# Performance work log

Hardware: AMD Instinct MI355X
Metric: run time of the kernel (lower is better)

## Reference

```python
import jax, jax.numpy as jnp
import numpy as np

N = 4096
IN_C = 256
F = 256          # num_filter
C = 40           # label_dim
KP1 = 3          # K+1 Chebyshev orders (K=2 hardcoded in forward)
E = 131072
TWO_PI = 2.0 * np.pi


def build_Lc(edges, q, edge_weight, n):
    """Conjugate of the normalized magnetic Laplacian (max_eigen=2 => L = -A_n * exp(i*Theta)).
    We return conj(L) because the original code swaps L.real/L.imag when feeding `process`,
    which is algebraically O_i = i * conj(T_i(L))."""
    row, col = edges[0], edges[1]
    A = jnp.zeros((n, n), jnp.float32).at[row, col].add(edge_weight)  # duplicates sum, as in coo_matrix
    A_sym = 0.5 * (A + A.T)
    d = A_sym.sum(axis=0)
    d = jnp.where(d == 0, 1.0, d)
    dinv = d ** -0.5
    A_n = dinv[:, None] * A_sym * dinv[None, :]
    Theta = TWO_PI * q * (A - A.T)
    # conj(L) = -A_n * exp(-i*Theta)
    return (-A_n).astype(jnp.complex64) * jnp.exp(-1j * Theta.astype(jnp.complex64))


def cheb_layer(Lc, Xr, Xi, W, b):
    """One ChebConv_Qin_Direct layer. Output = sum_i (i * T_i(conj(L)) @ Xc) @ W_i + bias,
    which reproduces the real/imag-swapped `process` of the original module."""
    Xc = (Xr + 1j * Xi).astype(jnp.complex64)      # [N, d]
    Z0 = Xc
    Z1 = Lc @ Xc                                   # sparse-equivalent spmm, dense here
    Z2 = 2.0 * (Lc @ Z1) - Z0                      # Chebyshev recursion T2 = 2 L T1 - T0
    Yc = 1j * (Z0 @ W[0].astype(jnp.complex64)
               + Z1 @ W[1].astype(jnp.complex64)
               + Z2 @ W[2].astype(jnp.complex64))  # [N, out]
    return Yc.real + b, Yc.imag + b


def setup_inputs() -> dict:
    key = jax.random.key(0)
    k = jax.random.split(key, 8)
    stdv1 = 1.0 / np.sqrt(F)
    return {
        "real": jax.random.normal(k[0], (N, IN_C), jnp.float32),
        "imag": jax.random.normal(k[1], (N, IN_C), jnp.float32),
        "edges": jax.random.randint(k[2], (2, E), 0, N),
        "q": jnp.float32(0.25),
        "edge_weight": jax.random.uniform(k[3], (E,), jnp.float32),
        "W1": jax.random.uniform(k[4], (KP1, IN_C, F), jnp.float32, -stdv1, stdv1),
        "b1": jnp.zeros((1, F), jnp.float32),
        "W2": jax.random.uniform(k[5], (KP1, F, F), jnp.float32, -stdv1, stdv1),
        "b2": jnp.zeros((1, F), jnp.float32),
        "Wc": jax.random.normal(k[6], (C, 2 * F), jnp.float32) * (1.0 / np.sqrt(2 * F)),
        "bc": jnp.zeros((C,), jnp.float32),
    }


def reference(real, imag, edges, q, edge_weight, W1, b1, W2, b2, Wc, bc):
    n = real.shape[0]
    Lc = build_Lc(edges, q, edge_weight, n)        # same L is rebuilt each layer in the original
    r, i = cheb_layer(Lc, real, imag, W1, b1)
    r, i = cheb_layer(Lc, r, i, W2, b2)            # activation=False, dropout=False
    x = jnp.concatenate([r, i], axis=-1)           # [N, 2F]
    logits = x @ Wc.T + bc                         # Conv1d(kernel_size=1) == linear
    return jax.nn.log_softmax(logits, axis=-1)     # [N, C]
```

## Files before the change

### kernel.cpp

```cpp
#include <hip/hip_runtime.h>
#include <cmath>

#define N_NODES 4096
#define FDIM    256
#define CDIM    40
#define NEDGE   131072
#define CAP     256
#define HBITS   20
#define HSIZE   (1 << HBITS)
#define TWO_PI_F 6.28318530717958647692f

typedef __bf16 bf16;
typedef __bf16 bf16x2 __attribute__((ext_vector_type(2)));
typedef __bf16 bf16x4 __attribute__((ext_vector_type(4)));
typedef __bf16 bf16x8 __attribute__((ext_vector_type(8)));
typedef float  f32x4  __attribute__((ext_vector_type(4)));

static constexpr size_t NF = (size_t)N_NODES * FDIM;

struct __align__(16) Entry { float lr, li; int col, pad; };

__device__ __forceinline__ void gld_lds16(const bf16* g, bf16* s) {
    __builtin_amdgcn_global_load_lds(
        (const __attribute__((address_space(1))) void*)g,
        (__attribute__((address_space(3))) void*)s,
        16, 0, 0);
}

__device__ __forceinline__ unsigned cell_hash(unsigned cell) {
    return (cell * 2654435761u) >> (32 - HBITS);
}

__global__ void hash_insert(const int* __restrict__ edges,
                            const float* __restrict__ ew,
                            int* __restrict__ hkey, float* __restrict__ hval,
                            float* __restrict__ rowsum, float* __restrict__ colsum) {
    int e = blockIdx.x * blockDim.x + threadIdx.x;
    if (e >= NEDGE) return;
    int r = edges[e], c = edges[NEDGE + e];
    float wv = ew[e];
    atomicAdd(rowsum + r, wv);
    atomicAdd(colsum + c, wv);
    unsigned cell = (unsigned)r * N_NODES + c;
    unsigned h = cell_hash(cell);
    for (;;) {
        int old = atomicCAS(hkey + h, 0, (int)(cell + 1));
        if (old == 0 || old == (int)(cell + 1)) { atomicAdd(hval + h, wv); break; }
        h = (h + 1) & (HSIZE - 1);
    }
}

__global__ __launch_bounds__(256) void hash_to_ell(
    const int* __restrict__ hkey, const float* __restrict__ hval,
    const float* __restrict__ rowsum, const float* __restrict__ colsum,
    const float* __restrict__ qptr,
    int* __restrict__ cnt, Entry* __restrict__ ent) {
    int h = blockIdx.x * 256 + threadIdx.x;
    int k = hkey[h];
    if (k == 0) return;
    unsigned cell = (unsigned)(k - 1);
    int i = cell >> 12, j = cell & 4095;
    float a = hval[h];
    float b = 0.f;
    bool mirror = false;
    if (i == j) { b = a; mirror = true; }
    else {
        unsigned mcell = (unsigned)j * N_NODES + i;
        unsigned hh = cell_hash(mcell);
        for (;;) {
            int kk = hkey[hh];
            if (kk == (int)(mcell + 1)) { b = hval[hh]; mirror = true; break; }
            if (kk == 0) break;
            hh = (hh + 1) & (HSIZE - 1);
        }
    }
    float di = 0.5f * (rowsum[i] + colsum[i]); if (di == 0.f) di = 1.f;
    float dj = 0.5f * (rowsum[j] + colsum[j]); if (dj == 0.f) dj = 1.f;
    float an = 0.5f * (a + b) / sqrtf(di * dj);
    float s, c;
    sincosf(TWO_PI_F * qptr[0] * (a - b), &s, &c);
    int pos = atomicAdd(cnt + i, 1);
    if (pos < CAP) {
        Entry en; en.lr = -an * c; en.li = an * s; en.col = j; en.pad = 0;
        ent[(size_t)i * CAP + pos] = en;
    }
    if (!mirror) {
        int pos2 = atomicAdd(cnt + j, 1);
        if (pos2 < CAP) {
            Entry en; en.lr = -an * c; en.li = -an * s; en.col = i; en.pad = 0;
            ent[(size_t)j * CAP + pos2] = en;
        }
    }
}

__global__ __launch_bounds__(256) void cast_in2(const float* __restrict__ Xr,
                                                const float* __restrict__ Xi,
                                                bf16* __restrict__ Xr16,
                                                bf16* __restrict__ Xi16,
                                                bf16* __restrict__ XC) {
    int idx = blockIdx.x * 256 + threadIdx.x;
    float vr = Xr[idx], vi = Xi[idx];
    Xr16[idx] = (bf16)vr; Xi16[idx] = (bf16)vi;
    bf16x2 p; p[0] = (bf16)vr; p[1] = (bf16)vi;
    ((bf16x2*)XC)[idx] = p;
}

#define NWT (256 * 768)
__global__ __launch_bounds__(256) void cast_weights(
    const float* __restrict__ W1, const float* __restrict__ W2,
    const float* __restrict__ Wc,
    bf16* __restrict__ W1t, bf16* __restrict__ W2t, bf16* __restrict__ Wcb) {
    int idx = blockIdx.x * 256 + threadIdx.x;
    if (idx < 2 * NWT) {
        const float* W = (idx < NWT) ? W1 : W2;
        bf16* Wt = (idx < NWT) ? W1t : W2t;
        int id = (idx < NWT) ? idx : idx - NWT;
        int nout = id / 768, kk = id - nout * 768;
        int o = kk >> 8, k = kk & 255;
        Wt[id] = (bf16)W[((size_t)o * 256 + k) * 256 + nout];
    } else {
        int id = idx - 2 * NWT;
        if (id < 48 * 512) {
            int row = id >> 9, k = id & 511;
            Wcb[id] = (row < CDIM) ? (bf16)Wc[row * 512 + k] : (bf16)0.f;
        }
    }
}

__global__ __launch_bounds__(256) void spmm_k(
    const int* __restrict__ cnt, const Entry* __restrict__ ent,
    const bf16* __restrict__ XC,
    const bf16* __restrict__ C0C,
    float alpha, float beta,
    bf16* __restrict__ Zr, bf16* __restrict__ Zi, bf16* __restrict__ ZC)
{
    __shared__ f32x4 redR[3][64];
    __shared__ f32x4 redI[3][64];

    const int wave = threadIdx.x >> 6, lane = threadIdx.x & 63;
    const int row = blockIdx.x;
    int n1 = cnt[row]; if (n1 > CAP) n1 = CAP;
    const Entry* erow = ent + (size_t)row * CAP;

    float ar[4] = {}, ai[4] = {};
    int e = wave;
    for (; e + 12 < n1; e += 16) {
        Entry e0 = erow[e];
        Entry e1 = erow[e + 4];
        Entry e2 = erow[e + 8];
        Entry e3 = erow[e + 12];
        bf16x8 x0 = *(const bf16x8*)&XC[(size_t)(e0.col & 4095) * 512 + lane * 8];
        bf16x8 x1 = *(const bf16x8*)&XC[(size_t)(e1.col & 4095) * 512 + lane * 8];
        bf16x8 x2 = *(const bf16x8*)&XC[(size_t)(e2.col & 4095) * 512 + lane * 8];
        bf16x8 x3 = *(const bf16x8*)&XC[(size_t)(e3.col & 4095) * 512 + lane * 8];
        #pragma unroll
        for (int c = 0; c < 4; ++c) {
            float xr, xi;
            xr = (float)x0[2 * c]; xi = (float)x0[2 * c + 1];
            ar[c] += e0.lr * xr - e0.li * xi;  ai[c] += e0.lr * xi + e0.li * xr;
            xr = (float)x1[2 * c]; xi = (float)x1[2 * c + 1];
            ar[c] += e1.lr * xr - e1.li * xi;  ai[c] += e1.lr * xi + e1.li * xr;
            xr = (float)x2[2 * c]; xi = (float)x2[2 * c + 1];
            ar[c] += e2.lr * xr - e2.li * xi;  ai[c] += e2.lr * xi + e2.li * xr;
            xr = (float)x3[2 * c]; xi = (float)x3[2 * c + 1];
            ar[c] += e3.lr * xr - e3.li * xi;  ai[c] += e3.lr * xi + e3.li * xr;
        }
    }
    for (; e < n1; e += 4) {
        Entry e0 = erow[e];
        bf16x8 x0 = *(const bf16x8*)&XC[(size_t)(e0.col & 4095) * 512 + lane * 8];
        #pragma unroll
        for (int c = 0; c < 4; ++c) {
            float xr0 = (float)x0[2 * c], xi0 = (float)x0[2 * c + 1];
            ar[c] += e0.lr * xr0 - e0.li * xi0;
            ai[c] += e0.lr * xi0 + e0.li * xr0;
        }
    }

    if (wave != 0) {
        f32x4 r, i;
        #pragma unroll
        for (int c = 0; c < 4; ++c) { r[c] = ar[c]; i[c] = ai[c]; }
        redR[wave - 1][lane] = r;
        redI[wave - 1][lane] = i;
    }
    __syncthreads();
    if (wave != 0) return;

    #pragma unroll
    for (int w = 0; w < 3; ++w) {
        f32x4 r = redR[w][lane], i = redI[w][lane];
        #pragma unroll
        for (int c = 0; c < 4; ++c) { ar[c] += r[c]; ai[c] += i[c]; }
    }

    float vr[4], vi[4];
    if (beta != 0.f) {
        bf16x8 c0 = *(const bf16x8*)&C0C[(size_t)row * 512 + lane * 8];
        #pragma unroll
        for (int c = 0; c < 4; ++c) {
            vr[c] = alpha * ar[c] + beta * (float)c0[2 * c];
            vi[c] = alpha * ai[c] + beta * (float)c0[2 * c + 1];
        }
    } else {
        #pragma unroll
        for (int c = 0; c < 4; ++c) { vr[c] = alpha * ar[c]; vi[c] = alpha * ai[c]; }
    }
    size_t base = (size_t)row * FDIM + lane * 4;
    bf16x4 pr, pi;
    #pragma unroll
    for (int c = 0; c < 4; ++c) { pr[c] = (bf16)vr[c]; pi[c] = (bf16)vi[c]; }
    *(bf16x4*)&Zr[base] = pr;
    *(bf16x4*)&Zi[base] = pi;
    if (ZC) {
        bf16x8 o;
        #pragma unroll
        for (int c = 0; c < 4; ++c) { o[2 * c] = pr[c]; o[2 * c + 1] = pi[c]; }
        *(bf16x8*)&ZC[(size_t)row * 512 + lane * 8] = o;
    }
}

__global__ __launch_bounds__(256) void wapply_mfma(
    const bf16* __restrict__ Z0r, const bf16* __restrict__ Z0i,
    const bf16* __restrict__ Z1r, const bf16* __restrict__ Z1i,
    const bf16* __restrict__ Z2r, const bf16* __restrict__ Z2i,
    const bf16* __restrict__ Wt,
    const float* __restrict__ bias,
    float* __restrict__ O32r, float* __restrict__ O32i,
    bf16* __restrict__ O16r_r, bf16* __restrict__ O16r_i,
    bf16* __restrict__ OC)
{
    __shared__ __align__(16) bf16 sZr[64 * 32];
    __shared__ __align__(16) bf16 sZi[64 * 32];
    __shared__ __align__(16) bf16 sW [64 * 32];

    const int tid  = threadIdx.x;
    const int wave = tid >> 6;
    const int lane = tid & 63;
    const int rowBase = blockIdx.y * 64;
    const int colBase = blockIdx.x * 64;

    const int srow = lane >> 2;
    const int skc  = (lane & 3) * 8;

    f32x4 accSr[2][2] = {}, accSi[2][2] = {};
    const int wm = wave & 1, wn = wave >> 1;
    const int fr = lane & 15;
    const int fk = (lane >> 4) * 8;

    for (int kb = 0; kb < 3 * FDIM; kb += 32) {
        int order = kb >> 8;
        int kloc  = kb & 255;
        if (wave == 0 || wave == 1) {
            const bf16* z;
            if (wave == 0) z = (order == 0) ? Z0r : (order == 1) ? Z1r : Z2r;
            else           z = (order == 0) ? Z0i : (order == 1) ? Z1i : Z2i;
            bf16* s = (wave == 0) ? sZr : sZi;
            const bf16* g = z + (size_t)(rowBase + srow) * FDIM + kloc + skc;
            #pragma unroll
            for (int t = 0; t < 4; ++t)
                gld_lds16(g + (size_t)t * 16 * FDIM, s + t * 512);
        } else if (wave == 2) {
            const bf16* g = Wt + (size_t)(colBase + srow) * 768 + kb + skc;
            #pragma unroll
            for (int t = 0; t < 4; ++t)
                gld_lds16(g + (size_t)t * 16 * 768, sW + t * 512);
        }
        __syncthreads();

        bf16x8 zr[2], zi[2], wv[2];
        #pragma unroll
        for (int m = 0; m < 2; ++m) {
            int r = wm * 32 + m * 16 + fr;
            zr[m] = *(const bf16x8*)&sZr[r * 32 + fk];
            zi[m] = *(const bf16x8*)&sZi[r * 32 + fk];
        }
        #pragma unroll
        for (int n = 0; n < 2; ++n) {
            int c = wn * 32 + n * 16 + fr;
            wv[n] = *(const bf16x8*)&sW[c * 32 + fk];
        }
        #pragma unroll
        for (int m = 0; m < 2; ++m)
            #pragma unroll
            for (int n = 0; n < 2; ++n) {
                accSr[m][n] = __builtin_amdgcn_mfma_f32_16x16x32_bf16(zr[m], wv[n], accSr[m][n], 0, 0, 0);
                accSi[m][n] = __builtin_amdgcn_mfma_f32_16x16x32_bf16(zi[m], wv[n], accSi[m][n], 0, 0, 0);
            }
        __syncthreads();
    }

    #pragma unroll
    for (int m = 0; m < 2; ++m)
        #pragma unroll
        for (int n = 0; n < 2; ++n) {
            int row0 = rowBase + wm * 32 + m * 16 + (lane >> 4) * 4;
            int col  = colBase + wn * 32 + n * 16 + (lane & 15);
            float bv = bias[col];
            #pragma unroll
            for (int r = 0; r < 4; ++r) {
                float vr = bv - accSi[m][n][r];
                float vi = bv + accSr[m][n][r];
                int row = row0 + r;
                size_t idx = (size_t)row * FDIM + col;
                if (O32r) {
                    O32r[idx] = vr; O32i[idx] = vi;
                }
                if (O16r_r) {
                    O16r_r[idx] = (bf16)vr; O16r_i[idx] = (bf16)vi;
                }
                if (OC) {
                    bf16x2 p; p[0] = (bf16)vr; p[1] = (bf16)vi;
                    ((bf16x2*)OC)[idx] = p;
                }
            }
        }
}

__global__ __launch_bounds__(256) void head_mfma(
    const bf16* __restrict__ Yrb,
    const bf16* __restrict__ Yib,
    const bf16* __restrict__ Wcb,
    const float* __restrict__ bc,
    float* __restrict__ out)
{
    __shared__ __align__(16) bf16 sY[64][72];
    __shared__ __align__(16) bf16 sW[48][72];
    __shared__ float sS[64][52];

    const int tid  = threadIdx.x;
    const int wave = tid >> 6;
    const int lane = tid & 63;
    const int r0 = blockIdx.x * 64;

    f32x4 acc[3] = {};

    for (int kb = 0; kb < 512; kb += 64) {
        const bf16* src = (kb < 256) ? Yrb : Yib;
        const int koff = kb & 255;
        #pragma unroll
        for (int e = 0; e < 2; ++e) {
            int idx = tid + e * 256;
            int rr = idx >> 3, kk = (idx & 7) * 8;
            *(bf16x8*)&sY[rr][kk] =
                *(const bf16x8*)&src[(size_t)(r0 + rr) * FDIM + koff + kk];
        }
        #pragma unroll
        for (int e = 0; e < 2; ++e) {
            int idx = tid + e * 256;
            if (idx < 384) {
                int rr = idx >> 3, kk = (idx & 7) * 8;
                *(bf16x8*)&sW[rr][kk] =
                    *(const bf16x8*)&Wcb[(size_t)rr * 512 + kb + kk];
            }
        }
        __syncthreads();
        #pragma unroll
        for (int ks = 0; ks < 2; ++ks) {
            bf16x8 a = *(const bf16x8*)&sY[wave * 16 + (lane & 15)][ks * 32 + (lane >> 4) * 8];
            #pragma unroll
            for (int n = 0; n < 3; ++n) {
                bf16x8 b = *(const bf16x8*)&sW[n * 16 + (lane & 15)][ks * 32 + (lane >> 4) * 8];
                acc[n] = __builtin_amdgcn_mfma_f32_16x16x32_bf16(a, b, acc[n], 0, 0, 0);
            }
        }
        __syncthreads();
    }

    #pragma unroll
    for (int n = 0; n < 3; ++n) {
        int col = n * 16 + (lane & 15);
        int rloc = wave * 16 + (lane >> 4) * 4;
        #pragma unroll
        for (int r = 0; r < 4; ++r)
            sS[rloc + r][col] = acc[n][r];
    }
    __syncthreads();

    if (tid < 64) {
        float mx = -INFINITY;
        #pragma unroll 8
        for (int c = 0; c < CDIM; ++c) {
            float lv = sS[tid][c] + bc[c];
            sS[tid][c] = lv;
            mx = fmaxf(mx, lv);
        }
        float se = 0.f;
        #pragma unroll 8
        for (int c = 0; c < CDIM; ++c) se += expf(sS[tid][c] - mx);
        float lse = mx + logf(se);
        #pragma unroll 8
        for (int c = 0; c < CDIM; ++c)
            out[(size_t)(r0 + tid) * CDIM + c] = sS[tid][c] - lse;
    }
}

extern "C" void kernel_launch(void* const* d_in, const int* in_sizes, int n_in,
                              void* d_out, int out_size, void* d_ws, size_t ws_size,
                              hipStream_t stream) {
    const float* real = (const float*)d_in[0];
    const float* imag = (const float*)d_in[1];
    const int*   edges = (const int*)d_in[2];
    const float* q    = (const float*)d_in[3];
    const float* ew   = (const float*)d_in[4];
    const float* W1   = (const float*)d_in[5];
    const float* b1   = (const float*)d_in[6];
    const float* W2   = (const float*)d_in[7];
    const float* b2   = (const float*)d_in[8];
    const float* Wc   = (const float*)d_in[9];
    const float* bc   = (const float*)d_in[10];
    float* out = (float*)d_out;

    char* w = (char*)d_ws;
    int*      hkey   = (int*)w;   w += (size_t)HSIZE * 4;
    float*    hval   = (float*)w; w += (size_t)HSIZE * 4;
    int*      cnt    = (int*)w;   w += N_NODES * 4;
    float*    rowsum = (float*)w; w += N_NODES * 4;
    float*    colsum = (float*)w; w += N_NODES * 4;
    size_t zero_bytes = (size_t)((char*)w - (char*)d_ws);
    Entry* ent  = (Entry*)w; w += (size_t)N_NODES * CAP * 16;
    bf16* Xr16 = (bf16*)w; w += NF * 2;
    bf16* Xi16 = (bf16*)w; w += NF * 2;
    bf16* XC   = (bf16*)w; w += NF * 4;
    bf16* Z1r  = (bf16*)w; w += NF * 2;
    bf16* Z1i  = (bf16*)w; w += NF * 2;
    bf16* Z1C  = (bf16*)w; w += NF * 4;
    bf16* Z2r  = (bf16*)w; w += NF * 2;
    bf16* Z2i  = (bf16*)w; w += NF * 2;
    float* Y1r32 = (float*)w; w += NF * 4;
    float* Y1i32 = (float*)w; w += NF * 4;
    bf16* Y1rb = (bf16*)w; w += NF * 2;
    bf16* Y1ib = (bf16*)w; w += NF * 2;
    bf16* Y1C  = (bf16*)w; w += NF * 4;
    bf16* Y2rb = (bf16*)w; w += NF * 2;
    bf16* Y2ib = (bf16*)w; w += NF * 2;
    bf16* W1t  = (bf16*)w; w += 256 * 768 * 2;
    bf16* W2t  = (bf16*)w; w += 256 * 768 * 2;
    bf16* Wcb  = (bf16*)w; w += 48 * 512 * 2;

    hipMemsetAsync(d_ws, 0, zero_bytes, stream);

    hash_insert<<<(NEDGE + 255) / 256, 256, 0, stream>>>(edges, ew, hkey, hval,
                                                         rowsum, colsum);
    hash_to_ell<<<HSIZE / 256, 256, 0, stream>>>(hkey, hval, rowsum, colsum,
                                                 q, cnt, ent);

    cast_in2<<<NF / 256, 256, 0, stream>>>(real, imag, Xr16, Xi16, XC);
    cast_weights<<<(2 * NWT + 48 * 512 + 255) / 256, 256, 0, stream>>>(
        W1, W2, Wc, W1t, W2t, Wcb);

    dim3 gW(FDIM / 64, N_NODES / 64);

    spmm_k<<<N_NODES, 256, 0, stream>>>(cnt, ent, XC, nullptr,
                                        1.f, 0.f, Z1r, Z1i, Z1C);
    spmm_k<<<N_NODES, 256, 0, stream>>>(cnt, ent, Z1C, XC,
                                        2.f, -1.f, Z2r, Z2i, nullptr);
    wapply_mfma<<<gW, 256, 0, stream>>>(Xr16, Xi16, Z1r, Z1i, Z2r, Z2i,
                                        W1t, b1,
                                        Y1r32, Y1i32,
                                        Y1rb, Y1ib,
                                        Y1C);

    spmm_k<<<N_NODES, 256, 0, stream>>>(cnt, ent, Y1C, nullptr,
                                        1.f, 0.f, Z1r, Z1i, Z1C);
    spmm_k<<<N_NODES, 256, 0, stream>>>(cnt, ent, Z1C, Y1C,
                                        2.f, -1.f, Z2r, Z2i, nullptr);
    wapply_mfma<<<gW, 256, 0, stream>>>(Y1rb, Y1ib, Z1r, Z1i, Z2r, Z2i,
                                        W2t, b2,
                                        nullptr, nullptr,
                                        Y2rb, Y2ib,
                                        nullptr);

    head_mfma<<<64, 256, 0, stream>>>(Y2rb, Y2ib, Wcb, bc, out);
}
```

Measured before the change: 275.0 us.

## Split SpMM rows into two feature panels, drop unused fp32 output, shrink hash

The SpMM kernel now launches two blocks per row, each handling half of the 512-wide complex feature vector with 8-byte loads per lane. This doubles the grid for more parallelism and latency hiding on the gather-bound step, at the cost of reading each row's edge list twice. The unused fp32 outputs of the first weight-apply kernel are removed, saving write traffic. The hash table is halved, which shrinks the memset and the hash_to_ell scan but raises the collision rate.

After: 319.2 us. 16.1% more time.

```diff
diff --git a/kernel.cpp b/kernel.cpp
--- a/kernel.cpp
+++ b/kernel.cpp
@@ -6,7 +6,7 @@
 #define CDIM    40
 #define NEDGE   131072
 #define CAP     256
-#define HBITS   20
+#define HBITS   19
 #define HSIZE   (1 << HBITS)
 #define TWO_PI_F 6.28318530717958647692f
 
@@ -14,6 +14,7 @@
 typedef __bf16 bf16x2 __attribute__((ext_vector_type(2)));
 typedef __bf16 bf16x4 __attribute__((ext_vector_type(4)));
 typedef __bf16 bf16x8 __attribute__((ext_vector_type(8)));
+typedef float  f32x2  __attribute__((ext_vector_type(2)));
 typedef float  f32x4  __attribute__((ext_vector_type(4)));
 
 static constexpr size_t NF = (size_t)N_NODES * FDIM;
@@ -134,27 +135,31 @@
     float alpha, float beta,
     bf16* __restrict__ Zr, bf16* __restrict__ Zi, bf16* __restrict__ ZC)
 {
-    __shared__ f32x4 redR[3][64];
-    __shared__ f32x4 redI[3][64];
+    __shared__ f32x2 redR[3][64];
+    __shared__ f32x2 redI[3][64];
 
     const int wave = threadIdx.x >> 6, lane = threadIdx.x & 63;
-    const int row = blockIdx.x;
+    const int bid = blockIdx.x;
+    const int row   = bid & (N_NODES - 1);
+    const int panel = bid >> 12;
     int n1 = cnt[row]; if (n1 > CAP) n1 = CAP;
     const Entry* erow = ent + (size_t)row * CAP;
 
-    float ar[4] = {}, ai[4] = {};
+    const int goff = panel * 256 + lane * 4;
+
+    float ar[2] = {}, ai[2] = {};
     int e = wave;
     for (; e + 12 < n1; e += 16) {
         Entry e0 = erow[e];
         Entry e1 = erow[e + 4];
         Entry e2 = erow[e + 8];
         Entry e3 = erow[e + 12];
-        bf16x8 x0 = *(const bf16x8*)&XC[(size_t)(e0.col & 4095) * 512 + lane * 8];
-        bf16x8 x1 = *(const bf16x8*)&XC[(size_t)(e1.col & 4095) * 512 + lane * 8];
-        bf16x8 x2 = *(const bf16x8*)&XC[(size_t)(e2.col & 4095) * 512 + lane * 8];
-        bf16x8 x3 = *(const bf16x8*)&XC[(size_t)(e3.col & 4095) * 512 + lane * 8];
-        #pragma unroll
-        for (int c = 0; c < 4; ++c) {
+        bf16x4 x0 = *(const bf16x4*)&XC[(size_t)(e0.col & 4095) * 512 + goff];
+        bf16x4 x1 = *(const bf16x4*)&XC[(size_t)(e1.col & 4095) * 512 + goff];
+        bf16x4 x2 = *(const bf16x4*)&XC[(size_t)(e2.col & 4095) * 512 + goff];
+        bf16x4 x3 = *(const bf16x4*)&XC[(size_t)(e3.col & 4095) * 512 + goff];
+        #pragma unroll
+        for (int c = 0; c < 2; ++c) {
             float xr, xi;
             xr = (float)x0[2 * c]; xi = (float)x0[2 * c + 1];
             ar[c] += e0.lr * xr - e0.li * xi;  ai[c] += e0.lr * xi + e0.li * xr;
@@ -168,9 +173,9 @@
     }
     for (; e < n1; e += 4) {
         Entry e0 = erow[e];
-        bf16x8 x0 = *(const bf16x8*)&XC[(size_t)(e0.col & 4095) * 512 + lane * 8];
-        #pragma unroll
-        for (int c = 0; c < 4; ++c) {
+        bf16x4 x0 = *(const bf16x4*)&XC[(size_t)(e0.col & 4095) * 512 + goff];
+        #pragma unroll
+        for (int c = 0; c < 2; ++c) {
             float xr0 = (float)x0[2 * c], xi0 = (float)x0[2 * c + 1];
             ar[c] += e0.lr * xr0 - e0.li * xi0;
             ai[c] += e0.lr * xi0 + e0.li * xr0;
@@ -178,9 +183,9 @@
     }
 
     if (wave != 0) {
-        f32x4 r, i;
-        #pragma unroll
-        for (int c = 0; c < 4; ++c) { r[c] = ar[c]; i[c] = ai[c]; }
+        f32x2 r, i;
+        #pragma unroll
+        for (int c = 0; c < 2; ++c) { r[c] = ar[c]; i[c] = ai[c]; }
         redR[wave - 1][lane] = r;
         redI[wave - 1][lane] = i;
     }
@@ -189,34 +194,34 @@
 
     #pragma unroll
     for (int w = 0; w < 3; ++w) {
-        f32x4 r = redR[w][lane], i = redI[w][lane];
-        #pragma unroll
-        for (int c = 0; c < 4; ++c) { ar[c] += r[c]; ai[c] += i[c]; }
-    }
-
-    float vr[4], vi[4];
+        f32x2 r = redR[w][lane], i = redI[w][lane];
+        #pragma unroll
+        for (int c = 0; c < 2; ++c) { ar[c] += r[c]; ai[c] += i[c]; }
+    }
+
+    float vr[2], vi[2];
     if (beta != 0.f) {
-        bf16x8 c0 = *(const bf16x8*)&C0C[(size_t)row * 512 + lane * 8];
-        #pragma unroll
-        for (int c = 0; c < 4; ++c) {
+        bf16x4 c0 = *(const bf16x4*)&C0C[(size_t)row * 512 + goff];
+        #pragma unroll
+        for (int c = 0; c < 2; ++c) {
             vr[c] = alpha * ar[c] + beta * (float)c0[2 * c];
             vi[c] = alpha * ai[c] + beta * (float)c0[2 * c + 1];
         }
     } else {
         #pragma unroll
-        for (int c = 0; c < 4; ++c) { vr[c] = alpha * ar[c]; vi[c] = alpha * ai[c]; }
-    }
-    size_t base = (size_t)row * FDIM + lane * 4;
-    bf16x4 pr, pi;
+        for (int c = 0; c < 2; ++c) { vr[c] = alpha * ar[c]; vi[c] = alpha * ai[c]; }
+    }
+    size_t base = (size_t)row * FDIM + panel * 128 + lane * 2;
+    bf16x2 pr, pi;
     #pragma unroll
-    for (int c = 0; c < 4; ++c) { pr[c] = (bf16)vr[c]; pi[c] = (bf16)vi[c]; }
-    *(bf16x4*)&Zr[base] = pr;
-    *(bf16x4*)&Zi[base] = pi;
+    for (int c = 0; c < 2; ++c) { pr[c] = (bf16)vr[c]; pi[c] = (bf16)vi[c]; }
+    *(bf16x2*)&Zr[base] = pr;
+    *(bf16x2*)&Zi[base] = pi;
     if (ZC) {
-        bf16x8 o;
-        #pragma unroll
-        for (int c = 0; c < 4; ++c) { o[2 * c] = pr[c]; o[2 * c + 1] = pi[c]; }
-        *(bf16x8*)&ZC[(size_t)row * 512 + lane * 8] = o;
+        bf16x4 o;
+        #pragma unroll
+        for (int c = 0; c < 2; ++c) { o[2 * c] = pr[c]; o[2 * c + 1] = pi[c]; }
+        *(bf16x4*)&ZC[(size_t)row * 512 + goff] = o;
     }
 }
 
@@ -226,7 +231,6 @@
     const bf16* __restrict__ Z2r, const bf16* __restrict__ Z2i,
     const bf16* __restrict__ Wt,
     const float* __restrict__ bias,
-    float* __restrict__ O32r, float* __restrict__ O32i,
     bf16* __restrict__ O16r_r, bf16* __restrict__ O16r_i,
     bf16* __restrict__ OC)
 {
@@ -303,9 +307,6 @@
                 float vi = bv + accSr[m][n][r];
                 int row = row0 + r;
                 size_t idx = (size_t)row * FDIM + col;
-                if (O32r) {
-                    O32r[idx] = vr; O32i[idx] = vi;
-                }
                 if (O16r_r) {
                     O16r_r[idx] = (bf16)vr; O16r_i[idx] = (bf16)vi;
                 }
@@ -427,8 +428,6 @@
     bf16* Z1C  = (bf16*)w; w += NF * 4;
     bf16* Z2r  = (bf16*)w; w += NF * 2;
     bf16* Z2i  = (bf16*)w; w += NF * 2;
-    float* Y1r32 = (float*)w; w += NF * 4;
-    float* Y1i32 = (float*)w; w += NF * 4;
     bf16* Y1rb = (bf16*)w; w += NF * 2;
     bf16* Y1ib = (bf16*)w; w += NF * 2;
     bf16* Y1C  = (bf16*)w; w += NF * 4;
@@ -450,24 +449,23 @@
         W1, W2, Wc, W1t, W2t, Wcb);
 
     dim3 gW(FDIM / 64, N_NODES / 64);
-
-    spmm_k<<<N_NODES, 256, 0, stream>>>(cnt, ent, XC, nullptr,
-                                        1.f, 0.f, Z1r, Z1i, Z1C);
-    spmm_k<<<N_NODES, 256, 0, stream>>>(cnt, ent, Z1C, XC,
-                                        2.f, -1.f, Z2r, Z2i, nullptr);
+    const int gS = 2 * N_NODES;
+
+    spmm_k<<<gS, 256, 0, stream>>>(cnt, ent, XC, nullptr,
+                                   1.f, 0.f, Z1r, Z1i, Z1C);
+    spmm_k<<<gS, 256, 0, stream>>>(cnt, ent, Z1C, XC,
+                                   2.f, -1.f, Z2r, Z2i, nullptr);
     wapply_mfma<<<gW, 256, 0, stream>>>(Xr16, Xi16, Z1r, Z1i, Z2r, Z2i,
                                         W1t, b1,
-                                        Y1r32, Y1i32,
                                         Y1rb, Y1ib,
                                         Y1C);
 
-    spmm_k<<<N_NODES, 256, 0, stream>>>(cnt, ent, Y1C, nullptr,
-                                        1.f, 0.f, Z1r, Z1i, Z1C);
-    spmm_k<<<N_NODES, 256, 0, stream>>>(cnt, ent, Z1C, Y1C,
-                                        2.f, -1.f, Z2r, Z2i, nullptr);
+    spmm_k<<<gS, 256, 0, stream>>>(cnt, ent, Y1C, nullptr,
+                                   1.f, 0.f, Z1r, Z1i, Z1C);
+    spmm_k<<<gS, 256, 0, stream>>>(cnt, ent, Z1C, Y1C,
+                                   2.f, -1.f, Z2r, Z2i, nullptr);
     wapply_mfma<<<gW, 256, 0, stream>>>(Y1rb, Y1ib, Z1r, Z1i, Z2r, Z2i,
                                         W2t, b2,
-                                        nullptr, nullptr,
                                         Y2rb, Y2ib,
                                         nullptr);
 
```
